# Kernel tuning notes

Measured on AMD Instinct MI355X. Metric: run time of the kernel, lower is better.

Reference implementation:

```python
import jax, jax.numpy as jnp
import numpy as np

B, S, D, H = 4, 2048, 1024, 16
DK = D // H

def setup_inputs() -> dict:
    key = jax.random.key(0)
    ks = jax.random.split(key, 11)
    std = 1.0 / np.sqrt(D)
    return {
        "q": jax.random.normal(ks[0], (B, S, D), jnp.float32),
        "k": jax.random.normal(ks[1], (B, S, D), jnp.float32),
        "v": jax.random.normal(ks[2], (B, S, D), jnp.float32),
        "Wq": jax.random.normal(ks[3], (D, D), jnp.float32) * std,
        "bq": jax.random.normal(ks[4], (D,), jnp.float32) * std,
        "Wk": jax.random.normal(ks[5], (D, D), jnp.float32) * std,
        "bk": jax.random.normal(ks[6], (D,), jnp.float32) * std,
        "Wv": jax.random.normal(ks[7], (D, D), jnp.float32) * std,
        "bv": jax.random.normal(ks[8], (D,), jnp.float32) * std,
        "Wo": jax.random.normal(ks[9], (D, D), jnp.float32) * std,
        "bo": jax.random.normal(ks[10], (D,), jnp.float32) * std,
    }

def reference(q, k, v, Wq, bq, Wk, bk, Wv, bv, Wo, bo):
    # Linear projections (torch nn.Linear: x @ W.T + b), split into heads
    def proj(x, W, b):
        y = jnp.einsum('bsd,ed->bse', x, W) + b          # [B,S,D]
        return y.reshape(B, S, H, DK).transpose(0, 2, 1, 3)  # [B,H,S,dk]
    qh = proj(q, Wq, bq)
    kh = proj(k, Wk, bk)
    vh = proj(v, Wv, bv)
    scale = 1.0 / np.sqrt(DK).astype(np.float32)
    scores = jnp.einsum('bhqd,bhkd->bhqk', qh, kh) * scale  # [B,H,S,S]
    attn = jax.nn.softmax(scores, axis=-1)
    # dropout is identity in eval mode
    out = jnp.einsum('bhqk,bhkd->bhqd', attn, vh)           # [B,H,S,dk]
    concat = out.transpose(0, 2, 1, 3).reshape(B, S, D)     # [B,S,D]
    return jnp.einsum('bsd,ed->bse', concat, Wo) + bo
```

## Files before the change

### kernel.cpp

```cpp
#include <hip/hip_runtime.h>
#include <hip/hip_bf16.h>
#include <cstdint>
#include <cstddef>

#define BB   4
#define SS   2048
#define DD   1024
#define HH   16
#define DKK  64
#define MM   (BB*SS)

typedef __bf16 bf16;
typedef __bf16 bf16x8 __attribute__((ext_vector_type(8)));
typedef __bf16 bf16x4 __attribute__((ext_vector_type(4)));
typedef float  f32x4  __attribute__((ext_vector_type(4)));

__device__ __forceinline__ f32x4 mfma16(bf16x8 a, bf16x8 b, f32x4 c) {
  return __builtin_amdgcn_mfma_f32_16x16x32_bf16(a, b, c, 0, 0, 0);
}

__device__ __forceinline__ void gload_lds16(const void* g, void* l) {
  __builtin_amdgcn_global_load_lds((const __attribute__((address_space(1))) void*)g,
                                   (__attribute__((address_space(3))) void*)l, 16, 0, 0);
}

__device__ __forceinline__ float fexp2(float x) {
#if __has_builtin(__builtin_amdgcn_exp2f)
  return __builtin_amdgcn_exp2f(x);
#else
  return exp2f(x);
#endif
}

__global__ void cvt3_bf16(const float* __restrict__ s0, const float* __restrict__ s1,
                          const float* __restrict__ s2, bf16* __restrict__ d0,
                          bf16* __restrict__ d1, bf16* __restrict__ d2, int n) {
  const int z = blockIdx.y;
  const float* in = (z == 0) ? s0 : (z == 1) ? s1 : s2;
  bf16* out = (z == 0) ? d0 : (z == 1) ? d1 : d2;
  int i = (blockIdx.x * blockDim.x + threadIdx.x) * 4;
  if (i >= n) return;
  float4 f = *(const float4*)(in + i);
  const float* fp = (const float*)&f;
  bf16x4 h;
#pragma unroll
  for (int j = 0; j < 4; j++) h[j] = (bf16)fp[j];
  *(bf16x4*)(out + i) = h;
}

__global__ void cvt_wcat(const float* __restrict__ in, bf16* __restrict__ out) {
  int i = (blockIdx.x * blockDim.x + threadIdx.x) * 4;
  float4 f = *(const float4*)(in + i);
  const float* fp = (const float*)&f;
  bf16x4 h, l;
#pragma unroll
  for (int j = 0; j < 4; j++) {
    h[j] = (bf16)fp[j];
    l[j] = (bf16)(fp[j] - (float)h[j]);
  }
  const int n_ = i >> 10, k_ = i & 1023;
  bf16* row = out + (size_t)n_ * 3072;
  *(bf16x4*)(row + k_)        = h;
  *(bf16x4*)(row + 1024 + k_) = l;
  *(bf16x4*)(row + 2048 + k_) = h;
}

template<int MODE>
__launch_bounds__(256)
__global__ void gemm_bt(const bf16* __restrict__ A, const bf16* __restrict__ Bw,
                        const float* __restrict__ bias, void* __restrict__ outp,
                        int K, float scale) {
  __shared__ bf16 As[2][128 * 32];
  __shared__ bf16 Bs[2][128 * 32];
  const int t = threadIdx.x, lane = t & 63, w = t >> 6;
  const int wr = w >> 1, wc = w & 1, l15 = lane & 15, l4 = lane >> 4;
  const int brow = blockIdx.y * 128, bcol = blockIdx.x * 128;
  const size_t Kb = (size_t)K * 2;
  const char* Ab = (const char*)A + (size_t)brow * Kb;
  const char* Bb = (const char*)Bw + (size_t)bcol * Kb;

  const int p0 = w * 2048 + lane * 16, p1 = p0 + 1024;
  const int r0 = p0 >> 6, r1 = p1 >> 6;
  const size_t sOff0 = (size_t)r0 * Kb + (size_t)((p0 & 63) ^ ((r0 & 3) << 4));
  const size_t sOff1 = (size_t)r1 * Kb + (size_t)((p1 & 63) ^ ((r1 & 3) << 4));

  const f32x4 zero4 = {0.f, 0.f, 0.f, 0.f};
  f32x4 acc[4][4];
#pragma unroll
  for (int i = 0; i < 4; i++)
#pragma unroll
    for (int j = 0; j < 4; j++) acc[i][j] = zero4;

  auto stage = [&](int buf, int k0) {
    const char* At = Ab + (size_t)k0 * 2;
    const char* Bt = Bb + (size_t)k0 * 2;
    char* ad = (char*)&As[buf][0];
    char* bd = (char*)&Bs[buf][0];
    gload_lds16(At + sOff0, ad + w * 2048);
    gload_lds16(At + sOff1, ad + w * 2048 + 1024);
    gload_lds16(Bt + sOff0, bd + w * 2048);
    gload_lds16(Bt + sOff1, bd + w * 2048 + 1024);
  };

  const int nk = K / 32;
  stage(0, 0);
  for (int tk = 0; tk < nk; ++tk) {
    const int buf = tk & 1;
    if (tk + 1 < nk) {
      stage(buf ^ 1, (tk + 1) * 32);
      asm volatile("s_waitcnt vmcnt(4)\ns_barrier" ::: "memory");
    } else {
      asm volatile("s_waitcnt vmcnt(0)\ns_barrier" ::: "memory");
    }
    const char* ab = (const char*)&As[buf][0];
    const char* bb = (const char*)&Bs[buf][0];
    bf16x8 af[4], bfr[4];
#pragma unroll
    for (int i = 0; i < 4; i++) {
      const int rr = wr * 64 + i * 16 + l15;
      af[i] = *(const bf16x8*)(ab + rr * 64 + ((l4 * 16) ^ ((rr & 3) << 4)));
    }
#pragma unroll
    for (int i = 0; i < 4; i++) {
      const int rr = wc * 64 + i * 16 + l15;
      bfr[i] = *(const bf16x8*)(bb + rr * 64 + ((l4 * 16) ^ ((rr & 3) << 4)));
    }
#pragma unroll
    for (int mi = 0; mi < 4; mi++)
#pragma unroll
      for (int ni = 0; ni < 4; ni++)
        acc[mi][ni] = mfma16(af[mi], bfr[ni], acc[mi][ni]);
    asm volatile("s_barrier" ::: "memory");
  }

#pragma unroll
  for (int mi = 0; mi < 4; mi++) {
    const int row0 = brow + wr * 64 + mi * 16 + l4 * 4;
#pragma unroll
    for (int ni = 0; ni < 4; ni++) {
      const int col = bcol + wc * 64 + ni * 16 + l15;
      if (MODE == 0) {
        const float bv = bias[col];
        bf16* outh = (bf16*)outp;
        const int h = col >> 6, dk = col & 63;
#pragma unroll
        for (int r = 0; r < 4; r++) {
          const int row = row0 + r;
          const int b_ = row >> 11, s_ = row & 2047;
          outh[(((size_t)b_ * HH + h) * SS + s_) * DKK + dk] =
              (bf16)((acc[mi][ni][r] + bv) * scale);
        }
      } else if (MODE == 1) {
        const float bv = bias[col];
        float* outf = (float*)outp;
#pragma unroll
        for (int r = 0; r < 4; r++)
          outf[(size_t)(row0 + r) * DD + col] = acc[mi][ni][r] + bv;
      } else {
        bf16* outT = (bf16*)outp;
        const int b_ = col >> 11, s_ = col & 2047;
#pragma unroll
        for (int r = 0; r < 4; r++) {
          const int row = row0 + r;
          outT[((size_t)b_ * 1024 + row) * 2048 + s_] = (bf16)(acc[mi][ni][r] + bias[row]);
        }
      }
    }
  }
}

__launch_bounds__(512)
__global__ void attn_fwd(const bf16* __restrict__ Qh, const bf16* __restrict__ Kh,
                         const bf16* __restrict__ VhT, bf16* __restrict__ Ccat) {
  __shared__ bf16 Ks[2][64 * 64];
  __shared__ bf16 Vs[2][64 * 64];
  __shared__ bf16 Pl[8][32 * 64];
  const int t = threadIdx.x, lane = t & 63, w = t >> 6;
  const int l15 = lane & 15, l4 = lane >> 4;
  const int id  = blockIdx.x;
  const int swz = (id & 7) * 64 + (id >> 3);
  const int bh = swz >> 3, qb = swz & 7;
  const int b_ = bh >> 4, h = bh & 15;
  const int q0 = qb * 256 + w * 32;
  const bf16* Qp = Qh + (size_t)bh * SS * DKK;
  const char* Kbase = (const char*)(Kh + (size_t)bh * SS * DKK);
  const char* Vbase = (const char*)(VhT + (size_t)bh * DKK * SS);

  const int p = w * 1024 + lane * 16;
  const int r_ = p >> 7;
  const int lo = (p & 127) ^ ((r_ & 7) << 4);
  const size_t kOff = (size_t)(p & ~127) + (size_t)lo;
  const size_t vOff = (size_t)r_ * (SS * 2) + (size_t)lo;

  bf16x8 qf[2][2];
#pragma unroll
  for (int mi = 0; mi < 2; mi++)
#pragma unroll
    for (int s = 0; s < 2; s++)
      qf[mi][s] = *(const bf16x8*)(Qp + (size_t)(q0 + mi * 16 + l15) * DKK + s * 32 + l4 * 8);

  const f32x4 zero4 = {0.f, 0.f, 0.f, 0.f};
  f32x4 o[2][4];
  float lsum[2][4];
#pragma unroll
  for (int mi = 0; mi < 2; mi++)
#pragma unroll
    for (int r = 0; r < 4; r++) lsum[mi][r] = 0.f;
#pragma unroll
  for (int mi = 0; mi < 2; mi++)
#pragma unroll
    for (int nd = 0; nd < 4; nd++) o[mi][nd] = zero4;

  auto stage = [&](int buf, int kt) {
    gload_lds16(Kbase + (size_t)kt * 128 + kOff, (char*)&Ks[buf][0] + w * 1024);
    gload_lds16(Vbase + (size_t)kt * 2 + vOff, (char*)&Vs[buf][0] + w * 1024);
  };

  char* pw = (char*)&Pl[w][0];
  stage(0, 0);
  for (int kt = 0; kt < SS; kt += 64) {
    const int buf = (kt >> 6) & 1;
    if (kt + 64 < SS) {
      stage(buf ^ 1, kt + 64);
      asm volatile("s_waitcnt vmcnt(2)\ns_barrier" ::: "memory");
    } else {
      asm volatile("s_waitcnt vmcnt(0)\ns_barrier" ::: "memory");
    }
    const char* kb = (const char*)&Ks[buf][0];
    const char* vb = (const char*)&Vs[buf][0];
    f32x4 sc[2][4];
#pragma unroll
    for (int mi = 0; mi < 2; mi++)
#pragma unroll
      for (int ni = 0; ni < 4; ni++) sc[mi][ni] = zero4;
#pragma unroll
    for (int s = 0; s < 2; s++) {
      bf16x8 kf[4];
#pragma unroll
      for (int ni = 0; ni < 4; ni++) {
        const int rr = ni * 16 + l15;
        kf[ni] = *(const bf16x8*)(kb + rr * 128 + ((s * 64 + l4 * 16) ^ ((rr & 7) << 4)));
      }
#pragma unroll
      for (int mi = 0; mi < 2; mi++)
#pragma unroll
        for (int ni = 0; ni < 4; ni++)
          sc[mi][ni] = mfma16(qf[mi][s], kf[ni], sc[mi][ni]);
    }
#pragma unroll
    for (int mi = 0; mi < 2; mi++)
#pragma unroll
      for (int r = 0; r < 4; r++) {
        const int pr = mi * 16 + l4 * 4 + r;
        char* prow = pw + pr * 128;
        const int sw = (pr & 7) << 4;
#pragma unroll
        for (int ni = 0; ni < 4; ni++) {
          const float pv = fexp2(sc[mi][ni][r]);
          lsum[mi][r] += pv;
          *(bf16*)(prow + ((2 * (ni * 16 + l15)) ^ sw)) = (bf16)pv;
        }
      }
#pragma unroll
    for (int s = 0; s < 2; s++) {
      bf16x8 pf[2], vf[4];
#pragma unroll
      for (int mi = 0; mi < 2; mi++) {
        const int rr = mi * 16 + l15;
        pf[mi] = *(const bf16x8*)(pw + rr * 128 + ((s * 64 + l4 * 16) ^ ((rr & 7) << 4)));
      }
#pragma unroll
      for (int nd = 0; nd < 4; nd++) {
        const int rr = nd * 16 + l15;
        vf[nd] = *(const bf16x8*)(vb + rr * 128 + ((s * 64 + l4 * 16) ^ ((rr & 7) << 4)));
      }
#pragma unroll
      for (int mi = 0; mi < 2; mi++)
#pragma unroll
        for (int nd = 0; nd < 4; nd++)
          o[mi][nd] = mfma16(pf[mi], vf[nd], o[mi][nd]);
    }
    asm volatile("s_barrier" ::: "memory");
  }
#pragma unroll
  for (int mi = 0; mi < 2; mi++)
#pragma unroll
    for (int r = 0; r < 4; r++) {
      float rs = lsum[mi][r];
      rs += __shfl_xor(rs, 1);
      rs += __shfl_xor(rs, 2);
      rs += __shfl_xor(rs, 4);
      rs += __shfl_xor(rs, 8);
      const float inv = 1.0f / rs;
      const int qg = q0 + mi * 16 + l4 * 4 + r;
      bf16* cp = Ccat + (size_t)(b_ * SS + qg) * 3072 + h * 64;
#pragma unroll
      for (int nd = 0; nd < 4; nd++) {
        const float val = o[mi][nd][r] * inv;
        const bf16 hi = (bf16)val;
        const bf16 lo2 = (bf16)(val - (float)hi);
        cp[nd * 16 + l15]        = hi;
        cp[1024 + nd * 16 + l15] = hi;
        cp[2048 + nd * 16 + l15] = lo2;
      }
    }
}

extern "C" void kernel_launch(void* const* d_in, const int* in_sizes, int n_in,
                              void* d_out, int out_size, void* d_ws, size_t ws_size,
                              hipStream_t stream) {
  const float* q  = (const float*)d_in[0];
  const float* k  = (const float*)d_in[1];
  const float* v  = (const float*)d_in[2];
  const float* Wq = (const float*)d_in[3];
  const float* bq = (const float*)d_in[4];
  const float* Wk = (const float*)d_in[5];
  const float* bk = (const float*)d_in[6];
  const float* Wv = (const float*)d_in[7];
  const float* bv = (const float*)d_in[8];
  const float* Wo = (const float*)d_in[9];
  const float* bo = (const float*)d_in[10];
  float* out = (float*)d_out;

  char* ws = (char*)d_ws;
  bf16* qb    = (bf16*)(ws + ((size_t)0   << 20));
  bf16* kb    = (bf16*)(ws + ((size_t)16  << 20));
  bf16* vb    = (bf16*)(ws + ((size_t)32  << 20));
  bf16* Wqb   = (bf16*)(ws + ((size_t)48  << 20));
  bf16* Wkb   = (bf16*)(ws + ((size_t)50  << 20));
  bf16* Wvb   = (bf16*)(ws + ((size_t)52  << 20));
  bf16* Wcat  = (bf16*)(ws + ((size_t)54  << 20));
  bf16* Qh    = (bf16*)(ws + ((size_t)60  << 20));
  bf16* Kh    = (bf16*)(ws + ((size_t)76  << 20));
  bf16* VhT   = (bf16*)(ws + ((size_t)92  << 20));
  bf16* Ccat  = (bf16*)(ws + ((size_t)0   << 20));

  const int nQ = MM * DD;
  const int nW = DD * DD;
  cvt3_bf16<<<dim3(nQ / 1024, 3), 256, 0, stream>>>(q, k, v, qb, kb, vb, nQ);
  cvt3_bf16<<<dim3(nW / 1024, 3), 256, 0, stream>>>(Wq, Wk, Wv, Wqb, Wkb, Wvb, nW);
  cvt_wcat<<<dim3(nW / 1024), 256, 0, stream>>>(Wo, Wcat);

  const float qscale = 0.125f * 1.44269504088896340736f;
  gemm_bt<0><<<dim3(DD / 128, MM / 128), 256, 0, stream>>>(qb, Wqb, bq, Qh, DD, qscale);
  gemm_bt<0><<<dim3(DD / 128, MM / 128), 256, 0, stream>>>(kb, Wkb, bk, Kh, DD, 1.0f);
  gemm_bt<2><<<dim3(MM / 128, DD / 128), 256, 0, stream>>>(Wvb, vb, bv, VhT, DD, 1.0f);

  attn_fwd<<<dim3(SS / 256 * BB * HH), 512, 0, stream>>>(Qh, Kh, VhT, Ccat);

  gemm_bt<1><<<dim3(DD / 128, MM / 128), 256, 0, stream>>>(Ccat, Wcat, bo, out, 3072, 1.0f);
}
```

Baseline: 436.8 us.

## Fuse QKV GEMMs into one launch and rewrite attention with 32x32 MFMA

Merges the three projection GEMMs into a single launch with block swizzling, and adds swizzled block ordering to the output GEMM. The attention kernel now uses 32x32x16 MFMA computing S^T, so P stays in registers: values are packed with cvt_pk_bf16 and permlane32_swap instead of being round-tripped through LDS. Block size drops to 256 threads and query tiles to 128, and the output stores are vectorized. The change removes LDS traffic and launch overhead, but adds register pressure and a dependence on exact lane-layout tricks.

```diff
diff --git a/kernel.cpp b/kernel.cpp
--- a/kernel.cpp
+++ b/kernel.cpp
@@ -14,9 +14,13 @@
 typedef __bf16 bf16x8 __attribute__((ext_vector_type(8)));
 typedef __bf16 bf16x4 __attribute__((ext_vector_type(4)));
 typedef float  f32x4  __attribute__((ext_vector_type(4)));
+typedef float  f32x16 __attribute__((ext_vector_type(16)));
 
 __device__ __forceinline__ f32x4 mfma16(bf16x8 a, bf16x8 b, f32x4 c) {
   return __builtin_amdgcn_mfma_f32_16x16x32_bf16(a, b, c, 0, 0, 0);
+}
+__device__ __forceinline__ f32x16 mfma32(bf16x8 a, bf16x8 b, f32x16 c) {
+  return __builtin_amdgcn_mfma_f32_32x32x16_bf16(a, b, c, 0, 0, 0);
 }
 
 __device__ __forceinline__ void gload_lds16(const void* g, void* l) {
@@ -30,6 +34,12 @@
 #else
   return exp2f(x);
 #endif
+}
+
+__device__ __forceinline__ unsigned cvt_pk_bf16(float a, float b) {
+  unsigned r;
+  asm("v_cvt_pk_bf16_f32 %0, %1, %2" : "=v"(r) : "v"(a), "v"(b));
+  return r;
 }
 
 __global__ void cvt3_bf16(const float* __restrict__ s0, const float* __restrict__ s1,
@@ -66,15 +76,14 @@
 }
 
 template<int MODE>
-__launch_bounds__(256)
-__global__ void gemm_bt(const bf16* __restrict__ A, const bf16* __restrict__ Bw,
-                        const float* __restrict__ bias, void* __restrict__ outp,
-                        int K, float scale) {
-  __shared__ bf16 As[2][128 * 32];
-  __shared__ bf16 Bs[2][128 * 32];
+__device__ __forceinline__ void gemm_core(const bf16* __restrict__ A,
+                                          const bf16* __restrict__ Bw,
+                                          const float* __restrict__ bias,
+                                          void* __restrict__ outp, int K, float scale,
+                                          int brow, int bcol,
+                                          bf16 (*As)[128 * 32], bf16 (*Bs)[128 * 32]) {
   const int t = threadIdx.x, lane = t & 63, w = t >> 6;
   const int wr = w >> 1, wc = w & 1, l15 = lane & 15, l4 = lane >> 4;
-  const int brow = blockIdx.y * 128, bcol = blockIdx.x * 128;
   const size_t Kb = (size_t)K * 2;
   const char* Ab = (const char*)A + (size_t)brow * Kb;
   const char* Bb = (const char*)Bw + (size_t)bcol * Kb;
@@ -169,140 +178,158 @@
   }
 }
 
-__launch_bounds__(512)
+__launch_bounds__(256)
+__global__ void gemm_qkv(const bf16* __restrict__ qb, const bf16* __restrict__ kb,
+                         const bf16* __restrict__ vb, const bf16* __restrict__ Wq,
+                         const bf16* __restrict__ Wk, const bf16* __restrict__ Wv,
+                         const float* __restrict__ bq, const float* __restrict__ bk,
+                         const float* __restrict__ bv, bf16* __restrict__ Qh,
+                         bf16* __restrict__ Kh, bf16* __restrict__ VhT, float qscale) {
+  __shared__ bf16 As[2][128 * 32];
+  __shared__ bf16 Bs[2][128 * 32];
+  const int id = blockIdx.x;
+  const int swz = (id & 7) * 192 + (id >> 3);
+  const int z = swz >> 9, rem = swz & 511;
+  const int x = rem >> 3, y = rem & 7;
+  if (z < 2) {
+    const bf16* Ap = z ? kb : qb;
+    const bf16* Wp = z ? Wk : Wq;
+    const float* bp = z ? bk : bq;
+    bf16* op = z ? Kh : Qh;
+    gemm_core<0>(Ap, Wp, bp, op, DD, z ? 1.0f : qscale, x * 128, y * 128, As, Bs);
+  } else {
+    gemm_core<2>(Wv, vb, bv, VhT, DD, 1.0f, y * 128, x * 128, As, Bs);
+  }
+}
+
+__launch_bounds__(256)
+__global__ void gemm_out(const bf16* __restrict__ Ccat, const bf16* __restrict__ Wcat,
+                         const float* __restrict__ bo, float* __restrict__ out) {
+  __shared__ bf16 As[2][128 * 32];
+  __shared__ bf16 Bs[2][128 * 32];
+  const int id = blockIdx.x;
+  const int swz = (id & 7) * 64 + (id >> 3);
+  gemm_core<1>(Ccat, Wcat, bo, out, 3072, 1.0f, (swz >> 3) * 128, (swz & 7) * 128, As, Bs);
+}
+
+__launch_bounds__(256)
 __global__ void attn_fwd(const bf16* __restrict__ Qh, const bf16* __restrict__ Kh,
                          const bf16* __restrict__ VhT, bf16* __restrict__ Ccat) {
   __shared__ bf16 Ks[2][64 * 64];
   __shared__ bf16 Vs[2][64 * 64];
-  __shared__ bf16 Pl[8][32 * 64];
   const int t = threadIdx.x, lane = t & 63, w = t >> 6;
-  const int l15 = lane & 15, l4 = lane >> 4;
+  const int l31 = lane & 31, hh = lane >> 5;
   const int id  = blockIdx.x;
-  const int swz = (id & 7) * 64 + (id >> 3);
-  const int bh = swz >> 3, qb = swz & 7;
-  const int b_ = bh >> 4, h = bh & 15;
-  const int q0 = qb * 256 + w * 32;
+  const int swz = (id & 7) * 128 + (id >> 3);
+  const int bh = swz >> 4, qb = swz & 15;
+  const int b_ = bh >> 4, head = bh & 15;
+  const int q0 = qb * 128 + w * 32;
   const bf16* Qp = Qh + (size_t)bh * SS * DKK;
   const char* Kbase = (const char*)(Kh + (size_t)bh * SS * DKK);
   const char* Vbase = (const char*)(VhT + (size_t)bh * DKK * SS);
 
-  const int p = w * 1024 + lane * 16;
-  const int r_ = p >> 7;
-  const int lo = (p & 127) ^ ((r_ & 7) << 4);
-  const size_t kOff = (size_t)(p & ~127) + (size_t)lo;
-  const size_t vOff = (size_t)r_ * (SS * 2) + (size_t)lo;
-
-  bf16x8 qf[2][2];
-#pragma unroll
-  for (int mi = 0; mi < 2; mi++)
-#pragma unroll
-    for (int s = 0; s < 2; s++)
-      qf[mi][s] = *(const bf16x8*)(Qp + (size_t)(q0 + mi * 16 + l15) * DKK + s * 32 + l4 * 8);
-
-  const f32x4 zero4 = {0.f, 0.f, 0.f, 0.f};
-  f32x4 o[2][4];
-  float lsum[2][4];
-#pragma unroll
-  for (int mi = 0; mi < 2; mi++)
-#pragma unroll
-    for (int r = 0; r < 4; r++) lsum[mi][r] = 0.f;
-#pragma unroll
-  for (int mi = 0; mi < 2; mi++)
-#pragma unroll
-    for (int nd = 0; nd < 4; nd++) o[mi][nd] = zero4;
+  const int p0 = w * 2048 + lane * 16, p1 = p0 + 1024;
+  const int r0 = p0 >> 7, r1 = p1 >> 7;
+  const int lo0 = (p0 & 127) ^ ((r0 & 7) << 4), lo1 = (p1 & 127) ^ ((r1 & 7) << 4);
+  const size_t kOff0 = (size_t)(p0 & ~127) + lo0;
+  const size_t kOff1 = (size_t)(p1 & ~127) + lo1;
+  const size_t vOff0 = (size_t)r0 * (SS * 2) + lo0;
+  const size_t vOff1 = (size_t)r1 * (SS * 2) + lo1;
+
+  bf16x8 qreg[4];
+  {
+    const char* qrow = (const char*)Qp + (size_t)(q0 + l31) * 128 + hh * 16;
+#pragma unroll
+    for (int c = 0; c < 4; c++) qreg[c] = *(const bf16x8*)(qrow + c * 32);
+  }
+
+  f32x16 zero16;
+#pragma unroll
+  for (int i = 0; i < 16; i++) zero16[i] = 0.f;
+  f32x16 ot[2];
+  ot[0] = zero16; ot[1] = zero16;
+  float lsum = 0.f;
 
   auto stage = [&](int buf, int kt) {
-    gload_lds16(Kbase + (size_t)kt * 128 + kOff, (char*)&Ks[buf][0] + w * 1024);
-    gload_lds16(Vbase + (size_t)kt * 2 + vOff, (char*)&Vs[buf][0] + w * 1024);
+    gload_lds16(Kbase + (size_t)kt * 128 + kOff0, (char*)&Ks[buf][0] + (p0 & ~1023) + (p0 & 1023 & ~0));
+    gload_lds16(Kbase + (size_t)kt * 128 + kOff1, (char*)&Ks[buf][0] + w * 2048 + 1024);
+    gload_lds16(Vbase + (size_t)kt * 2 + vOff0, (char*)&Vs[buf][0] + w * 2048);
+    gload_lds16(Vbase + (size_t)kt * 2 + vOff1, (char*)&Vs[buf][0] + w * 2048 + 1024);
   };
 
-  char* pw = (char*)&Pl[w][0];
-  stage(0, 0);
+  auto stage2 = [&](int buf, int kt) {
+    gload_lds16(Kbase + (size_t)kt * 128 + kOff0, (char*)&Ks[buf][0] + w * 2048);
+    gload_lds16(Kbase + (size_t)kt * 128 + kOff1, (char*)&Ks[buf][0] + w * 2048 + 1024);
+    gload_lds16(Vbase + (size_t)kt * 2 + vOff0, (char*)&Vs[buf][0] + w * 2048);
+    gload_lds16(Vbase + (size_t)kt * 2 + vOff1, (char*)&Vs[buf][0] + w * 2048 + 1024);
+  };
+
+  stage2(0, 0);
   for (int kt = 0; kt < SS; kt += 64) {
     const int buf = (kt >> 6) & 1;
     if (kt + 64 < SS) {
-      stage(buf ^ 1, kt + 64);
-      asm volatile("s_waitcnt vmcnt(2)\ns_barrier" ::: "memory");
+      stage2(buf ^ 1, kt + 64);
+      asm volatile("s_waitcnt vmcnt(4)\ns_barrier" ::: "memory");
     } else {
       asm volatile("s_waitcnt vmcnt(0)\ns_barrier" ::: "memory");
     }
-    const char* kb = (const char*)&Ks[buf][0];
-    const char* vb = (const char*)&Vs[buf][0];
-    f32x4 sc[2][4];
-#pragma unroll
-    for (int mi = 0; mi < 2; mi++)
-#pragma unroll
-      for (int ni = 0; ni < 4; ni++) sc[mi][ni] = zero4;
-#pragma unroll
-    for (int s = 0; s < 2; s++) {
-      bf16x8 kf[4];
-#pragma unroll
-      for (int ni = 0; ni < 4; ni++) {
-        const int rr = ni * 16 + l15;
-        kf[ni] = *(const bf16x8*)(kb + rr * 128 + ((s * 64 + l4 * 16) ^ ((rr & 7) << 4)));
+    const char* kbp = (const char*)&Ks[buf][0];
+    const char* vbp = (const char*)&Vs[buf][0];
+#pragma unroll
+    for (int kb = 0; kb < 2; kb++) {
+      f32x16 st;
+#pragma unroll
+      for (int c = 0; c < 4; c++) {
+        const int rr = kb * 32 + l31;
+        bf16x8 kf = *(const bf16x8*)(kbp + rr * 128 + ((c * 32 + hh * 16) ^ ((rr & 7) << 4)));
+        st = (c == 0) ? mfma32(kf, qreg[0], zero16) : mfma32(kf, qreg[c], st);
       }
-#pragma unroll
-      for (int mi = 0; mi < 2; mi++)
-#pragma unroll
-        for (int ni = 0; ni < 4; ni++)
-          sc[mi][ni] = mfma16(qf[mi][s], kf[ni], sc[mi][ni]);
-    }
-#pragma unroll
-    for (int mi = 0; mi < 2; mi++)
-#pragma unroll
-      for (int r = 0; r < 4; r++) {
-        const int pr = mi * 16 + l4 * 4 + r;
-        char* prow = pw + pr * 128;
-        const int sw = (pr & 7) << 4;
-#pragma unroll
-        for (int ni = 0; ni < 4; ni++) {
-          const float pv = fexp2(sc[mi][ni][r]);
-          lsum[mi][r] += pv;
-          *(bf16*)(prow + ((2 * (ni * 16 + l15)) ^ sw)) = (bf16)pv;
+      float pe[16];
+#pragma unroll
+      for (int r = 0; r < 16; r++) { pe[r] = fexp2(st[r]); lsum += pe[r]; }
+      unsigned pk[8];
+#pragma unroll
+      for (int g = 0; g < 8; g++) pk[g] = cvt_pk_bf16(pe[2 * g], pe[2 * g + 1]);
+      asm volatile("v_permlane32_swap_b32 %0, %1" : "+v"(pk[0]), "+v"(pk[2]));
+      asm volatile("v_permlane32_swap_b32 %0, %1" : "+v"(pk[1]), "+v"(pk[3]));
+      asm volatile("v_permlane32_swap_b32 %0, %1" : "+v"(pk[4]), "+v"(pk[6]));
+      asm volatile("v_permlane32_swap_b32 %0, %1" : "+v"(pk[5]), "+v"(pk[7]));
+#pragma unroll
+      for (int ci = 0; ci < 2; ci++) {
+        union { unsigned u[4]; bf16x8 v; } pu;
+        pu.u[0] = pk[ci * 4 + 0]; pu.u[1] = pk[ci * 4 + 1];
+        pu.u[2] = pk[ci * 4 + 2]; pu.u[3] = pk[ci * 4 + 3];
+#pragma unroll
+        for (int db = 0; db < 2; db++) {
+          const int rr = db * 32 + l31;
+          bf16x8 vf = *(const bf16x8*)(vbp + rr * 128 +
+                        ((kb * 64 + ci * 32 + hh * 16) ^ ((rr & 7) << 4)));
+          ot[db] = mfma32(vf, pu.v, ot[db]);
         }
       }
-#pragma unroll
-    for (int s = 0; s < 2; s++) {
-      bf16x8 pf[2], vf[4];
-#pragma unroll
-      for (int mi = 0; mi < 2; mi++) {
-        const int rr = mi * 16 + l15;
-        pf[mi] = *(const bf16x8*)(pw + rr * 128 + ((s * 64 + l4 * 16) ^ ((rr & 7) << 4)));
+    }
+    asm volatile("s_barrier" ::: "memory");
+  }
+
+  lsum += __shfl_xor(lsum, 32);
+  const float inv = 1.0f / lsum;
+  const int qg = q0 + l31;
+  bf16* cp = Ccat + (size_t)(b_ * SS + qg) * 3072 + head * 64;
+#pragma unroll
+  for (int db = 0; db < 2; db++)
+#pragma unroll
+    for (int g = 0; g < 4; g++) {
+      bf16x4 hi4, lo4;
+#pragma unroll
+      for (int r3 = 0; r3 < 4; r3++) {
+        const float val = ot[db][g * 4 + r3] * inv;
+        hi4[r3] = (bf16)val;
+        lo4[r3] = (bf16)(val - (float)hi4[r3]);
       }
-#pragma unroll
-      for (int nd = 0; nd < 4; nd++) {
-        const int rr = nd * 16 + l15;
-        vf[nd] = *(const bf16x8*)(vb + rr * 128 + ((s * 64 + l4 * 16) ^ ((rr & 7) << 4)));
-      }
-#pragma unroll
-      for (int mi = 0; mi < 2; mi++)
-#pragma unroll
-        for (int nd = 0; nd < 4; nd++)
-          o[mi][nd] = mfma16(pf[mi], vf[nd], o[mi][nd]);
-    }
-    asm volatile("s_barrier" ::: "memory");
-  }
-#pragma unroll
-  for (int mi = 0; mi < 2; mi++)
-#pragma unroll
-    for (int r = 0; r < 4; r++) {
-      float rs = lsum[mi][r];
-      rs += __shfl_xor(rs, 1);
-      rs += __shfl_xor(rs, 2);
-      rs += __shfl_xor(rs, 4);
-      rs += __shfl_xor(rs, 8);
-      const float inv = 1.0f / rs;
-      const int qg = q0 + mi * 16 + l4 * 4 + r;
-      bf16* cp = Ccat + (size_t)(b_ * SS + qg) * 3072 + h * 64;
-#pragma unroll
-      for (int nd = 0; nd < 4; nd++) {
-        const float val = o[mi][nd][r] * inv;
-        const bf16 hi = (bf16)val;
-        const bf16 lo2 = (bf16)(val - (float)hi);
-        cp[nd * 16 + l15]        = hi;
-        cp[1024 + nd * 16 + l15] = hi;
-        cp[2048 + nd * 16 + l15] = lo2;
-      }
+      const int d0 = db * 32 + g * 8 + hh * 4;
+      *(bf16x4*)(cp + d0)        = hi4;
+      *(bf16x4*)(cp + 1024 + d0) = hi4;
+      *(bf16x4*)(cp + 2048 + d0) = lo4;
     }
 }
 
@@ -342,11 +369,10 @@
   cvt_wcat<<<dim3(nW / 1024), 256, 0, stream>>>(Wo, Wcat);
 
   const float qscale = 0.125f * 1.44269504088896340736f;
-  gemm_bt<0><<<dim3(DD / 128, MM / 128), 256, 0, stream>>>(qb, Wqb, bq, Qh, DD, qscale);
-  gemm_bt<0><<<dim3(DD / 128, MM / 128), 256, 0, stream>>>(kb, Wkb, bk, Kh, DD, 1.0f);
-  gemm_bt<2><<<dim3(MM / 128, DD / 128), 256, 0, stream>>>(Wvb, vb, bv, VhT, DD, 1.0f);
-
-  attn_fwd<<<dim3(SS / 256 * BB * HH), 512, 0, stream>>>(Qh, Kh, VhT, Ccat);
-
-  gemm_bt<1><<<dim3(DD / 128, MM / 128), 256, 0, stream>>>(Ccat, Wcat, bo, out, 3072, 1.0f);
-}
+  gemm_qkv<<<dim3(1536), 256, 0, stream>>>(qb, kb, vb, Wqb, Wkb, Wvb,
+                                           bq, bk, bv, Qh, Kh, VhT, qscale);
+
+  attn_fwd<<<dim3(1024), 256, 0, stream>>>(Qh, Kh, VhT, Ccat);
+
+  gemm_out<<<dim3(512), 256, 0, stream>>>(Ccat, Wcat, bo, out);
+}
```

New measurement: 423.7 us. 3.0% less time.
